# Performance work log

Hardware: AMD Instinct MI355X
Metric: run time of the kernel (lower is better)

Reference implementation:

```python
import jax, jax.numpy as jnp
import numpy as np

N, F, E, B, D = 100000, 256, 128, 10000, 32
GAMMA, ZETA = -0.1, 1.1  # hard-concrete stretch params of L0Dense


def setup_inputs() -> dict:
    key = jax.random.key(0)
    ks = jax.random.split(key, 12)
    return {
        "nodes": jax.random.randint(ks[0], (B,), 0, N),
        "neigh_idx": jax.random.randint(ks[1], (B, D), 0, N),
        "neigh_mask": jax.random.bernoulli(ks[2], 0.9, (B, D)),
        "feature": jax.random.normal(ks[3], (N, F), jnp.float32),
        "W": jax.random.normal(ks[4], (F, E), jnp.float32) * 0.05,
        "b": jnp.zeros((E,), jnp.float32),
        "qz_loga": jax.random.normal(ks[5], (F,), jnp.float32),
        "att1_w": jax.random.normal(ks[6], (2 * E, E), jnp.float32) * 0.05,
        "att1_b": jnp.zeros((E,), jnp.float32),
        "att2_w": jax.random.normal(ks[7], (E, E), jnp.float32) * 0.05,
        "att2_b": jnp.zeros((E,), jnp.float32),
        "att3_w": jax.random.normal(ks[8], (E, 1), jnp.float32) * 0.05,
        "att3_b": jnp.zeros((1,), jnp.float32),
    }


def reference(nodes, neigh_idx, neigh_mask, feature, W, b, qz_loga,
              att1_w, att1_b, att2_w, att2_b, att3_w, att3_b):
    # L0Dense, deterministic (eval) hard-concrete gate on input dims
    z = jnp.clip(jax.nn.sigmoid(qz_loga) * (ZETA - GAMMA) + GAMMA, 0.0, 1.0)
    We = W * z[:, None]                                  # [F, E]

    node_feat = feature[nodes] @ We + b                   # [B, E]
    neigh_feat = feature[neigh_idx] @ We + b              # [B, D, E]

    # GraphRec-style attention MLP over (neighbor, center) pairs
    h = jnp.concatenate(
        [neigh_feat, jnp.broadcast_to(node_feat[:, None, :], neigh_feat.shape)],
        axis=-1)                                          # [B, D, 2E]
    h = jax.nn.relu(h @ att1_w + att1_b)
    h = jax.nn.relu(h @ att2_w + att2_b)
    scores = (h @ att3_w + att3_b)[..., 0]                # [B, D]
    scores = jnp.where(neigh_mask, scores, -1e30)
    att = jax.nn.softmax(scores, axis=-1)                 # [B, D]

    agg = jnp.einsum('bd,bde->be', att, neigh_feat)       # weighted sum
    has_neigh = neigh_mask.any(axis=-1, keepdims=True)
    return jnp.where(has_neigh, agg, node_feat)           # n==0 fallback
```

## Files before the change

### kernel.cpp

```cpp
#include <hip/hip_runtime.h>
#include <hip/hip_bf16.h>
#include <math.h>

#define NN 100000
#define FF 256
#define EE 128
#define BB_ 10000
#define DD 32

typedef __attribute__((ext_vector_type(8))) short short8;
typedef __attribute__((ext_vector_type(4))) float f32x4;

__device__ __forceinline__ short f2bf(float f) {
  __hip_bfloat16 h = __float2bfloat16(f);
  union { __hip_bfloat16 h; short s; } u; u.h = h;
  return u.s;
}
__device__ __forceinline__ float bf2f(short s) {
  union { unsigned u; float f; } v;
  v.u = ((unsigned)(unsigned short)s) << 16;
  return v.f;
}

__global__ __launch_bounds__(256) void k_prep(
    const float* __restrict__ W, const float* __restrict__ qz,
    const float* __restrict__ a1w, const float* __restrict__ a2w,
    const float* __restrict__ bb,
    float* __restrict__ Wef32, short* __restrict__ BT2,
    short* __restrict__ a1wTc, short* __restrict__ w2T,
    float* __restrict__ bias2) {
  int i = blockIdx.x * 256 + threadIdx.x;
  if (i < 32768) {
    int f = i >> 7, e = i & 127;
    float g = qz[f];
    float s = 1.0f / (1.0f + expf(-g));
    float z = fminf(fmaxf(s * 1.2f - 0.1f, 0.0f), 1.0f);
    float v = W[f * 128 + e] * z;
    Wef32[f * 128 + e] = v;
    BT2[e * 256 + f] = f2bf(v);
  } else if (i < 49152) {
    int t = i - 32768; int n = t >> 7, k = t & 127;
    a1wTc[n * 128 + k] = f2bf(a1w[(128 + k) * 128 + n]);
  } else if (i < 65536) {
    int t = i - 49152; int n = t >> 7, k = t & 127;
    w2T[n * 128 + k] = f2bf(a2w[k * 128 + n]);
  } else if (i < 65664) {
    bias2[i - 65536] = bb[i - 65536];
  }
}

__global__ __launch_bounds__(256) void k_compose(
    const float* __restrict__ Wef32, const float* __restrict__ a1w,
    const float* __restrict__ a1b, const float* __restrict__ bb,
    short* __restrict__ BT2, float* __restrict__ bias2) {
  const int n = blockIdx.x;
  const int f = threadIdx.x;
  float s = 0.f;
  for (int e = 0; e < 128; ++e)
    s = fmaf(a1w[e * 128 + n], Wef32[f * 128 + e], s);
  BT2[(size_t)(128 + n) * 256 + f] = f2bf(s);
  if (f == 0) {
    float by = a1b[n];
    for (int e = 0; e < 128; ++e) by = fmaf(bb[e], a1w[e * 128 + n], by);
    bias2[128 + n] = by;
  }
}

__global__ __launch_bounds__(512) void k_xy(
    const float* __restrict__ feat, const short* __restrict__ BT2,
    const float* __restrict__ bias2, short* __restrict__ XY, int M) {
  __shared__ short As[128 * 256];
  const int tid = threadIdx.x;
  const int mb = blockIdx.x * 128;
  const int wave = tid >> 6, lane = tid & 63;
  const int wr = wave >> 2, wn = wave & 3;
  const int l15 = lane & 15, lg = lane >> 4;

#pragma unroll
  for (int s = 0; s < 8; ++s) {
    int q = tid + s * 512;
    int row = q >> 5, c = q & 31;
    int grow = mb + row;
    if (grow >= M) grow = M - 1;
    const float* ap = feat + (size_t)grow * 256 + c * 8;
    float4 f0 = *(const float4*)ap;
    float4 f1 = *(const float4*)(ap + 4);
    short8 av;
    av[0] = f2bf(f0.x); av[1] = f2bf(f0.y);
    av[2] = f2bf(f0.z); av[3] = f2bf(f0.w);
    av[4] = f2bf(f1.x); av[5] = f2bf(f1.y);
    av[6] = f2bf(f1.z); av[7] = f2bf(f1.w);
    *(short8*)(As + row * 256 + 8 * (c ^ (row & 7))) = av;
  }
  __syncthreads();

  f32x4 acc[4][4];
#pragma unroll
  for (int i = 0; i < 4; ++i)
#pragma unroll
    for (int j = 0; j < 4; ++j) acc[i][j] = (f32x4){0.f, 0.f, 0.f, 0.f};

  const short* bbase = BT2 + (size_t)(wn * 64 + l15) * 256;
#pragma unroll
  for (int ks = 0; ks < 8; ++ks) {
    const int cc = ks * 4 + lg;
    short8 af[4], bf4[4];
#pragma unroll
    for (int i = 0; i < 4; ++i) {
      int r = wr * 64 + i * 16 + l15;
      af[i] = *(short8*)(As + r * 256 + 8 * (cc ^ (r & 7)));
    }
#pragma unroll
    for (int j = 0; j < 4; ++j)
      bf4[j] = *(const short8*)(bbase + j * 16 * 256 + cc * 8);
    __builtin_amdgcn_s_setprio(1);
#pragma unroll
    for (int i = 0; i < 4; ++i)
#pragma unroll
      for (int j = 0; j < 4; ++j)
        acc[i][j] = __builtin_amdgcn_mfma_f32_16x16x32_bf16(
            af[i], bf4[j], acc[i][j], 0, 0, 0);
    __builtin_amdgcn_s_setprio(0);
  }

  float bv4[4];
#pragma unroll
  for (int j = 0; j < 4; ++j) bv4[j] = bias2[wn * 64 + j * 16 + l15];
#pragma unroll
  for (int i = 0; i < 4; ++i) {
#pragma unroll
    for (int r = 0; r < 4; ++r) {
      int row = mb + wr * 64 + i * 16 + lg * 4 + r;
      if (row < M) {
#pragma unroll
        for (int j = 0; j < 4; ++j) {
          int col = wn * 64 + j * 16 + l15;
          XY[(size_t)row * 256 + col] = f2bf(acc[i][j][r] + bv4[j]);
        }
      }
    }
  }
}

template <int K, int LDA, int LDC, bool AF32, bool OUTBF16>
__global__ __launch_bounds__(256) void k_mm(
    const void* __restrict__ Ap, const short* __restrict__ BT,
    const float* __restrict__ bias, const int* __restrict__ idx,
    void* __restrict__ Cp, int M) {
  __shared__ short As[128 * 64];
  __shared__ short Bs[128 * 64];
  const int tid = threadIdx.x;
  const int mb = blockIdx.x * 128;
  const int col0 = blockIdx.y * 128;
  const int wave = tid >> 6, lane = tid & 63;
  const int wr = wave >> 1, wc = wave & 1;
  const int l15 = lane & 15, lg = lane >> 4;

  size_t abase[4];
#pragma unroll
  for (int s = 0; s < 4; ++s) {
    int row = (tid + s * 256) >> 3;
    int grow = mb + row;
    int gr = 0;
    if (grow < M) gr = idx ? idx[grow] : grow;
    abase[s] = (size_t)gr * LDA;
  }

  f32x4 acc[4][4];
#pragma unroll
  for (int i = 0; i < 4; ++i)
#pragma unroll
    for (int j = 0; j < 4; ++j) acc[i][j] = (f32x4){0.f, 0.f, 0.f, 0.f};

  for (int k0 = 0; k0 < K; k0 += 64) {
#pragma unroll
    for (int s = 0; s < 4; ++s) {
      int q = tid + s * 256;
      int row = q >> 3, c = q & 7;
      short8 av;
      if (AF32) {
        const float* ap = (const float*)Ap + abase[s] + k0 + c * 8;
        float4 f0 = *(const float4*)ap;
        float4 f1 = *(const float4*)(ap + 4);
        av[0] = f2bf(f0.x); av[1] = f2bf(f0.y);
        av[2] = f2bf(f0.z); av[3] = f2bf(f0.w);
        av[4] = f2bf(f1.x); av[5] = f2bf(f1.y);
        av[6] = f2bf(f1.z); av[7] = f2bf(f1.w);
      } else {
        av = *(const short8*)((const short*)Ap + abase[s] + k0 + c * 8);
      }
      *(short8*)(As + row * 64 + 8 * (c ^ (row & 7))) = av;
      short8 bv = *(const short8*)(BT + (size_t)(col0 + row) * K + k0 + c * 8);
      *(short8*)(Bs + row * 64 + 8 * (c ^ (row & 7))) = bv;
    }
    __syncthreads();
#pragma unroll
    for (int ks = 0; ks < 2; ++ks) {
      int c = ks * 4 + lg;
      short8 af[4], bfv[4];
#pragma unroll
      for (int i = 0; i < 4; ++i) {
        int r = wr * 64 + i * 16 + l15;
        af[i] = *(short8*)(As + r * 64 + 8 * (c ^ (r & 7)));
        int n = wc * 64 + i * 16 + l15;
        bfv[i] = *(short8*)(Bs + n * 64 + 8 * (c ^ (n & 7)));
      }
#pragma unroll
      for (int i = 0; i < 4; ++i)
#pragma unroll
        for (int j = 0; j < 4; ++j)
          acc[i][j] = __builtin_amdgcn_mfma_f32_16x16x32_bf16(
              af[i], bfv[j], acc[i][j], 0, 0, 0);
    }
    __syncthreads();
  }

  float bv4[4];
#pragma unroll
  for (int j = 0; j < 4; ++j) {
    int col = wc * 64 + j * 16 + l15;
    bv4[j] = bias ? bias[col0 + col] : 0.f;
  }
#pragma unroll
  for (int i = 0; i < 4; ++i) {
#pragma unroll
    for (int r = 0; r < 4; ++r) {
      int row = mb + wr * 64 + i * 16 + lg * 4 + r;
      if (row < M) {
#pragma unroll
        for (int j = 0; j < 4; ++j) {
          int col = wc * 64 + j * 16 + l15;
          float v = acc[i][j][r] + bv4[j];
          if (OUTBF16)
            ((short*)Cp)[(size_t)row * LDC + col0 + col] = f2bf(v);
          else
            ((float*)Cp)[(size_t)row * LDC + col0 + col] = v;
        }
      }
    }
  }
}

__global__ __launch_bounds__(256) void k_attn4(
    const short* __restrict__ XY, const float* __restrict__ P,
    const int* __restrict__ nodes, const int* __restrict__ nidx,
    const int* __restrict__ nmask, const short* __restrict__ w2T,
    const float* __restrict__ b2, const float* __restrict__ w3,
    const float* __restrict__ b3, float* __restrict__ out) {
  __shared__ int ni_s[4][32];
  __shared__ float sc_s[4][32];
  __shared__ float att_s[4][32];
  const int tid = threadIdx.x;
  const int wave = tid >> 6, lane = tid & 63;
  const int b = blockIdx.x * 4 + wave;
  const int l15 = lane & 15, lg = lane >> 4;

  if (lane < 32) ni_s[wave][lane] = nidx[b * DD + lane];

  const int m = nmask[(size_t)b * DD + (lane & 31)];
  const int nid0 = ni_s[wave][l15];
  const int nid1 = ni_s[wave][16 + l15];
  const short* yr0 = XY + (size_t)nid0 * 256 + 128;
  const short* yr1 = XY + (size_t)nid1 * 256 + 128;
  short8 y0v[4], y1v[4];
#pragma unroll
  for (int ks = 0; ks < 4; ++ks) {
    const int k0 = ks * 32 + lg * 8;
    y0v[ks] = *(const short8*)(yr0 + k0);
    y1v[ks] = *(const short8*)(yr1 + k0);
  }
  unsigned xv[32];
#pragma unroll
  for (int d = 0; d < 32; ++d)
    xv[d] = *(const unsigned*)(XY + (size_t)ni_s[wave][d] * 256 + 2 * lane);

  const float* pr = P + (size_t)b * EE;

  f32x4 acc[2][8];
#pragma unroll
  for (int i = 0; i < 2; ++i)
#pragma unroll
    for (int j = 0; j < 8; ++j) acc[i][j] = (f32x4){0.f, 0.f, 0.f, 0.f};

#pragma unroll
  for (int ks = 0; ks < 4; ++ks) {
    const int k0 = ks * 32 + lg * 8;
    float4 pa = *(const float4*)(pr + k0);
    float4 pb = *(const float4*)(pr + k0 + 4);
    float pf[8] = {pa.x, pa.y, pa.z, pa.w, pb.x, pb.y, pb.z, pb.w};
    short8 a0, a1;
#pragma unroll
    for (int e = 0; e < 8; ++e) {
      a0[e] = f2bf(fmaxf(bf2f(y0v[ks][e]) + pf[e], 0.f));
      a1[e] = f2bf(fmaxf(bf2f(y1v[ks][e]) + pf[e], 0.f));
    }
    short8 bfv[8];
#pragma unroll
    for (int j = 0; j < 8; ++j)
      bfv[j] = *(const short8*)(w2T + (size_t)(j * 16 + l15) * EE + k0);
    __builtin_amdgcn_s_setprio(1);
#pragma unroll
    for (int j = 0; j < 8; ++j) {
      acc[0][j] = __builtin_amdgcn_mfma_f32_16x16x32_bf16(a0, bfv[j],
                                                          acc[0][j], 0, 0, 0);
      acc[1][j] = __builtin_amdgcn_mfma_f32_16x16x32_bf16(a1, bfv[j],
                                                          acc[1][j], 0, 0, 0);
    }
    __builtin_amdgcn_s_setprio(0);
  }

  float b2v[8], w3v[8];
#pragma unroll
  for (int j = 0; j < 8; ++j) {
    int col = j * 16 + l15;
    b2v[j] = b2[col];
    w3v[j] = w3[col];
  }
  float part[2][4];
#pragma unroll
  for (int i = 0; i < 2; ++i)
#pragma unroll
    for (int r = 0; r < 4; ++r) {
      float s = 0.f;
#pragma unroll
      for (int j = 0; j < 8; ++j)
        s += fmaxf(acc[i][j][r] + b2v[j], 0.f) * w3v[j];
      part[i][r] = s;
    }
#pragma unroll
  for (int off = 1; off <= 8; off <<= 1) {
#pragma unroll
    for (int i = 0; i < 2; ++i)
#pragma unroll
      for (int r = 0; r < 4; ++r) part[i][r] += __shfl_xor(part[i][r], off);
  }
  if (l15 == 0) {
#pragma unroll
    for (int i = 0; i < 2; ++i)
#pragma unroll
      for (int r = 0; r < 4; ++r)
        sc_s[wave][i * 16 + lg * 4 + r] = part[i][r];
  }

  const int row = lane & 31;
  float s = sc_s[wave][row] + b3[0];
  if (!m) s = -1e30f;
  float mx = s;
#pragma unroll
  for (int off = 1; off <= 16; off <<= 1) mx = fmaxf(mx, __shfl_xor(mx, off));
  float e = expf(s - mx);
  float sum = e;
#pragma unroll
  for (int off = 1; off <= 16; off <<= 1) sum += __shfl_xor(sum, off);
  if (lane < 32) att_s[wave][row] = e / sum;
  const bool has = (__ballot(m != 0) != 0ull);

  float a0 = 0.f, a1 = 0.f;
  if (has) {
#pragma unroll
    for (int d = 0; d < 32; ++d) {
      float a = att_s[wave][d];
      a0 += a * bf2f((short)(xv[d] & 0xffffu));
      a1 += a * bf2f((short)(xv[d] >> 16));
    }
  } else {
    const short* xr = XY + (size_t)nodes[b] * 256;
    unsigned x2 = *(const unsigned*)(xr + 2 * lane);
    a0 = bf2f((short)(x2 & 0xffffu));
    a1 = bf2f((short)(x2 >> 16));
  }
  *(float2*)(out + (size_t)b * EE + 2 * lane) = make_float2(a0, a1);
}

extern "C" void kernel_launch(void* const* d_in, const int* in_sizes, int n_in,
                              void* d_out, int out_size, void* d_ws,
                              size_t ws_size, hipStream_t stream) {
  const int* nodes = (const int*)d_in[0];
  const int* nidx = (const int*)d_in[1];
  const int* nmask = (const int*)d_in[2];
  const float* feature = (const float*)d_in[3];
  const float* W = (const float*)d_in[4];
  const float* bb = (const float*)d_in[5];
  const float* qz = (const float*)d_in[6];
  const float* a1w = (const float*)d_in[7];
  const float* a1b = (const float*)d_in[8];
  const float* a2w = (const float*)d_in[9];
  const float* a2b = (const float*)d_in[10];
  const float* a3w = (const float*)d_in[11];
  const float* a3b = (const float*)d_in[12];
  float* out = (float*)d_out;

  char* ws = (char*)d_ws;
  short* BT2   = (short*)(ws);
  float* Wef32 = (float*)(ws + 131072);
  short* a1wTc = (short*)(ws + 262144);
  short* w2T   = (short*)(ws + 294912);
  float* bias2 = (float*)(ws + 327680);
  short* XYb   = (short*)(ws + 524288);
  float* Pv    = (float*)(ws + 524288 + 51200000);

  k_prep<<<257, 256, 0, stream>>>(W, qz, a1w, a2w, bb, Wef32, BT2, a1wTc, w2T,
                                  bias2);
  k_compose<<<128, 256, 0, stream>>>(Wef32, a1w, a1b, bb, BT2, bias2);
  k_xy<<<(NN + 127) / 128, 512, 0, stream>>>(feature, BT2, bias2, XYb, NN);
  k_mm<128, 256, 128, false, false><<<dim3((BB_ + 127) / 128, 1), 256, 0,
                                      stream>>>(XYb, a1wTc, nullptr, nodes, Pv,
                                                BB_);
  k_attn4<<<BB_ / 4, 256, 0, stream>>>(XYb, Pv, nodes, nidx, nmask, w2T, a2b,
                                       a3w, a3b, out);
}
```

Baseline: 139.5 us.

## Stream feature tiles into LDS via global_load_lds and keep B fragments in registers

```diff
diff --git a/kernel.cpp b/kernel.cpp
--- a/kernel.cpp
+++ b/kernel.cpp
@@ -20,6 +20,12 @@
   union { unsigned u; float f; } v;
   v.u = ((unsigned)(unsigned short)s) << 16;
   return v.f;
+}
+
+__device__ __forceinline__ void gll16(const float* g, float* lds) {
+  __builtin_amdgcn_global_load_lds(
+      (const __attribute__((address_space(1))) unsigned int*)g,
+      (__attribute__((address_space(3))) unsigned int*)lds, 16, 0, 0);
 }
 
 __global__ __launch_bounds__(256) void k_prep(
@@ -66,31 +72,30 @@
   }
 }
 
-__global__ __launch_bounds__(512) void k_xy(
+__global__ __launch_bounds__(256, 2) void k_xy(
     const float* __restrict__ feat, const short* __restrict__ BT2,
     const float* __restrict__ bias2, short* __restrict__ XY, int M) {
-  __shared__ short As[128 * 256];
+  __shared__ float As[64 * 256];
   const int tid = threadIdx.x;
-  const int mb = blockIdx.x * 128;
+  const int mb = blockIdx.x * 64;
   const int wave = tid >> 6, lane = tid & 63;
-  const int wr = wave >> 2, wn = wave & 3;
+  const int wn = wave;
   const int l15 = lane & 15, lg = lane >> 4;
 
-#pragma unroll
-  for (int s = 0; s < 8; ++s) {
-    int q = tid + s * 512;
-    int row = q >> 5, c = q & 31;
-    int grow = mb + row;
+  short8 bfr[8][4];
+#pragma unroll
+  for (int ks = 0; ks < 8; ++ks)
+#pragma unroll
+    for (int j = 0; j < 4; ++j)
+      bfr[ks][j] = *(const short8*)(BT2 +
+          (size_t)(wn * 64 + j * 16 + l15) * 256 + (ks * 4 + lg) * 8);
+
+#pragma unroll
+  for (int it = 0; it < 16; ++it) {
+    int r = it * 4 + wave;
+    int grow = mb + r;
     if (grow >= M) grow = M - 1;
-    const float* ap = feat + (size_t)grow * 256 + c * 8;
-    float4 f0 = *(const float4*)ap;
-    float4 f1 = *(const float4*)(ap + 4);
-    short8 av;
-    av[0] = f2bf(f0.x); av[1] = f2bf(f0.y);
-    av[2] = f2bf(f0.z); av[3] = f2bf(f0.w);
-    av[4] = f2bf(f1.x); av[5] = f2bf(f1.y);
-    av[6] = f2bf(f1.z); av[7] = f2bf(f1.w);
-    *(short8*)(As + row * 256 + 8 * (c ^ (row & 7))) = av;
+    gll16(feat + (size_t)grow * 256 + lane * 4, As + r * 256);
   }
   __syncthreads();
 
@@ -100,27 +105,27 @@
 #pragma unroll
     for (int j = 0; j < 4; ++j) acc[i][j] = (f32x4){0.f, 0.f, 0.f, 0.f};
 
-  const short* bbase = BT2 + (size_t)(wn * 64 + l15) * 256;
 #pragma unroll
   for (int ks = 0; ks < 8; ++ks) {
-    const int cc = ks * 4 + lg;
-    short8 af[4], bf4[4];
+    const int kg = ks * 4 + lg;
 #pragma unroll
     for (int i = 0; i < 4; ++i) {
-      int r = wr * 64 + i * 16 + l15;
-      af[i] = *(short8*)(As + r * 256 + 8 * (cc ^ (r & 7)));
-    }
-#pragma unroll
-    for (int j = 0; j < 4; ++j)
-      bf4[j] = *(const short8*)(bbase + j * 16 * 256 + cc * 8);
-    __builtin_amdgcn_s_setprio(1);
-#pragma unroll
-    for (int i = 0; i < 4; ++i)
+      const int r = i * 16 + l15;
+      const float* ap = As + r * 256 + kg * 8;
+      float4 flo = *(const float4*)ap;
+      float4 fhi = *(const float4*)(ap + 4);
+      short8 af;
+      af[0] = f2bf(flo.x); af[1] = f2bf(flo.y);
+      af[2] = f2bf(flo.z); af[3] = f2bf(flo.w);
+      af[4] = f2bf(fhi.x); af[5] = f2bf(fhi.y);
+      af[6] = f2bf(fhi.z); af[7] = f2bf(fhi.w);
+      __builtin_amdgcn_s_setprio(1);
 #pragma unroll
       for (int j = 0; j < 4; ++j)
         acc[i][j] = __builtin_amdgcn_mfma_f32_16x16x32_bf16(
-            af[i], bf4[j], acc[i][j], 0, 0, 0);
-    __builtin_amdgcn_s_setprio(0);
+            af, bfr[ks][j], acc[i][j], 0, 0, 0);
+      __builtin_amdgcn_s_setprio(0);
+    }
   }
 
   float bv4[4];
@@ -130,7 +135,7 @@
   for (int i = 0; i < 4; ++i) {
 #pragma unroll
     for (int r = 0; r < 4; ++r) {
-      int row = mb + wr * 64 + i * 16 + lg * 4 + r;
+      int row = mb + i * 16 + lg * 4 + r;
       if (row < M) {
 #pragma unroll
         for (int j = 0; j < 4; ++j) {
@@ -402,7 +407,7 @@
   k_prep<<<257, 256, 0, stream>>>(W, qz, a1w, a2w, bb, Wef32, BT2, a1wTc, w2T,
                                   bias2);
   k_compose<<<128, 256, 0, stream>>>(Wef32, a1w, a1b, bb, BT2, bias2);
-  k_xy<<<(NN + 127) / 128, 512, 0, stream>>>(feature, BT2, bias2, XYb, NN);
+  k_xy<<<(NN + 63) / 64, 256, 0, stream>>>(feature, BT2, bias2, XYb, NN);
   k_mm<128, 256, 128, false, false><<<dim3((BB_ + 127) / 128, 1), 256, 0,
                                       stream>>>(XYb, a1wTc, nullptr, nodes, Pv,
                                                 BB_);
```

Result: slower. 173.0 us (+24.0%).
